# Kernel optimization log

Measured on AMD Instinct MI355X. Metric: run time of the kernel, lower is better.

## Reference

```python
import jax, jax.numpy as jnp
import numpy as np

B, H, W, D = 8, 32, 32, 384      # batch, height, width, channels (=dim)
E, HID, O = 8, 1536, 384         # num_experts, mlp hidden (dim*4), out_dim
TOP_K = 2


def setup_inputs() -> dict:
    key = jax.random.key(0)
    ks = jax.random.split(key, 5)
    x = jax.random.normal(ks[0], (B, H, W, D), dtype=jnp.float32)
    # router (noise_linear unused: eval path, train=False)
    Wg = 0.02 * jax.random.normal(ks[1], (D, E), dtype=jnp.float32)
    bg = jnp.zeros((E,), dtype=jnp.float32)
    # per-expert MLP params stacked along expert axis
    W1 = 0.02 * jax.random.normal(ks[2], (E, D, HID), dtype=jnp.float32)
    b1 = jnp.zeros((E, HID), dtype=jnp.float32)
    W2 = 0.02 * jax.random.normal(ks[3], (E, HID, O), dtype=jnp.float32)
    b2 = jnp.zeros((E, O), dtype=jnp.float32)
    return {"x": x, "Wg": Wg, "bg": bg, "W1": W1, "b1": b1, "W2": W2, "b2": b2}


def reference(x, Wg, bg, W1, b1, W2, b2):
    # --- NoisyTopkRouter (eval: train=False -> no noise branch) ---
    logits = jnp.einsum('bhwd,de->bhwe', x, Wg) + bg            # [B,H,W,E]
    _, top_idx = jax.lax.top_k(logits, TOP_K)                   # [B,H,W,K]
    # mask of selected experts; sparse logits = logits where selected, -inf else
    sel = jnp.sum(jax.nn.one_hot(top_idx, E, dtype=jnp.float32), axis=-2) > 0
    sparse_logits = jnp.where(sel, logits, -jnp.inf)
    gates = jax.nn.softmax(sparse_logits, axis=-1)              # zero on non-top-k

    # --- experts: since gate is exactly 0 off the top-k, the masked
    # gather-MLP-scatter loop equals a gate-weighted sum of all expert MLPs ---
    h = jnp.einsum('bhwd,edf->bhwef', x, W1) + b1               # [B,H,W,E,HID]
    h = jax.nn.gelu(h, approximate=False)                       # torch nn.GELU = exact
    y = jnp.einsum('bhwef,efo->bhweo', h, W2) + b2              # [B,H,W,E,O]
    out = jnp.einsum('bhweo,bhwe->bhwo', y, gates)              # [B,H,W,O]
    return out
```

## Files before the change

### kernel.cpp

```cpp
#include <hip/hip_runtime.h>
#include <cmath>

#define N_TOK 8192
#define DIM   384
#define NEXP  8
#define HID   1536
#define OUTD  384
#define CAP_MT 72
#define CAP_TOK 2304
#define CAP_TB 18

typedef __attribute__((ext_vector_type(8)))  __bf16 bf16x8;
typedef __attribute__((ext_vector_type(16))) float  f32x16;
typedef __attribute__((ext_vector_type(4)))  float  f32x4;
typedef __attribute__((ext_vector_type(8)))  unsigned short u16x8;

__device__ __forceinline__ unsigned short f2bf(float f) {
    unsigned u = __float_as_uint(f);
    u += 0x7FFF + ((u >> 16) & 1);
    return (unsigned short)(u >> 16);
}

__device__ __forceinline__ float bf2f(unsigned short s) {
    return __uint_as_float(((unsigned)s) << 16);
}

__device__ __forceinline__ float gelu_exact(float x) {
    return 0.5f * x * (1.0f + erff(x * 0.70710678118654752f));
}

__device__ __forceinline__ void cp16(const unsigned short* g, unsigned short* l) {
    __builtin_amdgcn_global_load_lds(
        (const __attribute__((address_space(1))) unsigned int*)g,
        (__attribute__((address_space(3))) unsigned int*)l, 16, 0, 0);
}

__global__ void swizzle_kernel(const float* __restrict__ W1, const float* __restrict__ W2,
                               unsigned short* __restrict__ w1s, unsigned short* __restrict__ w2s,
                               int* __restrict__ cnt) {
    if (blockIdx.x == 0 && threadIdx.x < NEXP) cnt[threadIdx.x] = 0;
    int gid = blockIdx.x * blockDim.x + threadIdx.x;
    const int T1 = NEXP * 48 * 24 * 64;
    const int T2 = NEXP * 12 * 96 * 64;
    const float* src; unsigned short* dst; int K, N, NT, KT, g;
    if (gid < T1)           { src = W1; dst = w1s; K = DIM; N = HID;  NT = 48; KT = 24; g = gid; }
    else if (gid < T1 + T2) { src = W2; dst = w2s; K = HID; N = OUTD; NT = 12; KT = 96; g = gid - T1; }
    else return;
    int l  = g & 63;
    int kt = (g >> 6) % KT;
    int nt = ((g >> 6) / KT) % NT;
    int e  = g / (64 * KT * NT);
    const float* s = src + ((size_t)e * K + kt * 16 + (l >> 5) * 8) * N + nt * 32 + (l & 31);
    unsigned short r[8];
    #pragma unroll
    for (int j = 0; j < 8; ++j) r[j] = f2bf(s[(size_t)j * N]);
    *(uint4*)(dst + (size_t)g * 8) = *(uint4*)r;
}

__global__ void router_kernel(const float* __restrict__ x, const float* __restrict__ Wg,
                              const float* __restrict__ bg, int* __restrict__ cnt,
                              int* __restrict__ btok, int* __restrict__ tokmap,
                              float* __restrict__ gmap) {
    __shared__ float WgL[NEXP * DIM];
    __shared__ int lcnt[NEXP];
    __shared__ int lbase[NEXP];
    int tid = threadIdx.x;
    for (int i = tid; i < DIM * NEXP; i += 256) {
        int ch = i >> 3, e = i & 7;
        WgL[e * DIM + ch] = Wg[i];
    }
    if (tid < NEXP) lcnt[tid] = 0;
    __syncthreads();

    int tl  = tid >> 3;
    int seg = tid & 7;
    int t   = blockIdx.x * 32 + tl;

    float lg[NEXP] = {0.f, 0.f, 0.f, 0.f, 0.f, 0.f, 0.f, 0.f};
    const float* xr = x + (size_t)t * DIM;
    #pragma unroll
    for (int d4 = 0; d4 < 12; ++d4) {
        float4 v = *(const float4*)(xr + d4 * 32 + seg * 4);
        #pragma unroll
        for (int e = 0; e < NEXP; ++e) {
            float4 w = *(const float4*)&WgL[e * DIM + d4 * 32 + seg * 4];
            lg[e] += v.x * w.x + v.y * w.y + v.z * w.z + v.w * w.w;
        }
    }
    #pragma unroll
    for (int off = 1; off < 8; off <<= 1)
        #pragma unroll
        for (int e = 0; e < NEXP; ++e)
            lg[e] += __shfl_xor(lg[e], off);

    int p0 = 0, p1 = 0, i0 = 0, i1 = 0;
    float g0 = 0.f, g1 = 0.f;
    if (seg == 0) {
        float v0 = -INFINITY, v1 = -INFINITY;
        #pragma unroll
        for (int e = 0; e < NEXP; ++e) {
            float v = lg[e] + bg[e];
            if (v > v0)      { v1 = v0; i1 = i0; v0 = v; i0 = e; }
            else if (v > v1) { v1 = v;  i1 = e; }
        }
        float e1 = expf(v1 - v0);
        g0 = 1.f / (1.f + e1);
        g1 = e1  / (1.f + e1);
        p0 = atomicAdd(&lcnt[i0], 1);
        p1 = atomicAdd(&lcnt[i1], 1);
    }
    __syncthreads();
    if (tid < NEXP) lbase[tid] = atomicAdd(&cnt[tid], lcnt[tid]);
    __syncthreads();
    if (seg == 0) {
        int o0 = lbase[i0] + p0, o1 = lbase[i1] + p1;
        btok[i0 * N_TOK + o0] = t;
        btok[i1 * N_TOK + o1] = t;
        ((int4*)tokmap)[t] = make_int4(i0, o0, i1, o1);
        ((float2*)gmap)[t] = make_float2(g0, g1);
    }
}

__global__ void gather_kernel(const float* __restrict__ x, const int* __restrict__ cnt,
                              const int* __restrict__ btok, unsigned short* __restrict__ xg) {
    int mt = blockIdx.x, e = blockIdx.y;
    int cntE = cnt[e];
    if (mt * 32 >= cntE) return;
    int tid = threadIdx.x;
    int m = tid & 31, kt0 = tid >> 5;
    int pos = mt * 32 + m;
    int idx = (pos < cntE) ? pos : cntE - 1;
    int tok = btok[e * N_TOK + idx];
    const float* xr = x + (size_t)tok * DIM;
    #pragma unroll
    for (int kk = 0; kk < 3; ++kk) {
        int kt = kt0 + kk * 8;
        #pragma unroll
        for (int kh = 0; kh < 2; ++kh) {
            float4 v0 = *(const float4*)(xr + kt * 16 + kh * 8);
            float4 v1 = *(const float4*)(xr + kt * 16 + kh * 8 + 4);
            unsigned short rr[8];
            rr[0] = f2bf(v0.x); rr[1] = f2bf(v0.y); rr[2] = f2bf(v0.z); rr[3] = f2bf(v0.w);
            rr[4] = f2bf(v1.x); rr[5] = f2bf(v1.y); rr[6] = f2bf(v1.z); rr[7] = f2bf(v1.w);
            *(uint4*)(xg + (size_t)(((e * CAP_MT + mt) * 24 + kt) * 64 + kh * 32 + m) * 8) =
                *(uint4*)rr;
        }
    }
}

__global__ __launch_bounds__(256, 3) void gemm1_kernel(
        const unsigned short* __restrict__ xg, const unsigned short* __restrict__ w1s,
        const float* __restrict__ b1, const int* __restrict__ cnt,
        unsigned short* __restrict__ h) {
    int L = blockIdx.x;
    int e = L & 7;
    int r = L >> 3;
    int nb = r % 12;
    int tb = r / 12;
    int cntE = cnt[e];
    if (tb * 128 >= cntE) return;

    __shared__ unsigned short stg[32 * 512];

    int tid = threadIdx.x;
    int wave = tid >> 6, lane = tid & 63;
    int m31 = lane & 31, kh = lane >> 5;
    int wm = wave & 1, wn = wave >> 1;

    f32x16 acc[2][2];
    #pragma unroll
    for (int i = 0; i < 2; ++i)
        #pragma unroll
        for (int j = 0; j < 2; ++j)
            acc[i][j] = (f32x16){0.f,0.f,0.f,0.f,0.f,0.f,0.f,0.f,0.f,0.f,0.f,0.f,0.f,0.f,0.f,0.f};

    const unsigned short* xa = xg  + ((size_t)(e * CAP_MT + tb * 4) * 24) * 512;
    const unsigned short* wb = w1s + ((size_t)(e * 48 + nb * 4) * 24) * 512;

    const unsigned short* sbase = (wave < 2)
        ? xa + ((size_t)(wave * 2) * 24) * 512 + lane * 8
        : wb + ((size_t)((wave - 2) * 2) * 24) * 512 + lane * 8;
    unsigned short* dbase = &stg[wave * 8 * 512];

    for (int ks = 0; ks < 6; ++ks) {
        __syncthreads();
        const unsigned short* sk = sbase + ks * 2048;
        #pragma unroll
        for (int q = 0; q < 8; ++q)
            cp16(sk + (q >> 2) * (24 * 512) + (q & 3) * 512, dbase + q * 512);
        __syncthreads();
        #pragma unroll
        for (int kt = 0; kt < 4; ++kt) {
            bf16x8 a0 = *(const bf16x8*)&stg[((wm * 2 + 0) * 4 + kt) * 512 + lane * 8];
            bf16x8 a1 = *(const bf16x8*)&stg[((wm * 2 + 1) * 4 + kt) * 512 + lane * 8];
            bf16x8 b0 = *(const bf16x8*)&stg[(16 + (wn * 2 + 0) * 4 + kt) * 512 + lane * 8];
            bf16x8 b1v = *(const bf16x8*)&stg[(16 + (wn * 2 + 1) * 4 + kt) * 512 + lane * 8];
            acc[0][0] = __builtin_amdgcn_mfma_f32_32x32x16_bf16(a0, b0,  acc[0][0], 0, 0, 0);
            acc[0][1] = __builtin_amdgcn_mfma_f32_32x32x16_bf16(a0, b1v, acc[0][1], 0, 0, 0);
            acc[1][0] = __builtin_amdgcn_mfma_f32_32x32x16_bf16(a1, b0,  acc[1][0], 0, 0, 0);
            acc[1][1] = __builtin_amdgcn_mfma_f32_32x32x16_bf16(a1, b1v, acc[1][1], 0, 0, 0);
        }
    }

    __syncthreads();
    char* hw = (char*)&stg[wave * 4096];
    float bv0 = b1[e * HID + nb * 128 + wn * 64 + m31];
    float bv1 = b1[e * HID + nb * 128 + wn * 64 + 32 + m31];
    #pragma unroll
    for (int im = 0; im < 2; ++im)
        #pragma unroll
        for (int in = 0; in < 2; ++in) {
            float bv = in ? bv1 : bv0;
            #pragma unroll
            for (int rr = 0; rr < 16; ++rr) {
                int row = im * 32 + (rr & 3) + 8 * (rr >> 2) + 4 * kh;
                int col = in * 32 + m31;
                unsigned boff = (unsigned)(row * 128 + col * 2) ^ ((row & 7) << 4);
                *(unsigned short*)(hw + boff) = f2bf(gelu_exact(acc[im][in][rr] + bv));
            }
        }
    #pragma unroll
    for (int mtl = 0; mtl < 2; ++mtl)
        #pragma unroll
        for (int ktl = 0; ktl < 4; ++ktl) {
            int rowl = mtl * 32 + m31;
            int coll = ktl * 16 + kh * 8;
            unsigned boff = (unsigned)(rowl * 128 + coll * 2) ^ ((rowl & 7) << 4);
            uint4 v = *(const uint4*)(hw + boff);
            int mt = tb * 4 + wm * 2 + mtl;
            int kt = nb * 8 + wn * 4 + ktl;
            *(uint4*)(h + ((size_t)((e * CAP_MT + mt) * 96 + kt)) * 512 + lane * 8) = v;
        }
}

__global__ __launch_bounds__(512, 4) void gemm2_kernel(
        const unsigned short* __restrict__ h, const unsigned short* __restrict__ w2s,
        const int* __restrict__ cnt, unsigned short* __restrict__ yp) {
    int L = blockIdx.x;
    int e = L & 7;
    int r = L >> 3;
    int nb = r % 3;
    int tb = r / 3;
    int cntE = cnt[e];
    if (tb * 128 >= cntE) return;

    __shared__ unsigned short stg[32 * 512];

    int tid = threadIdx.x;
    int wave = tid >> 6, lane = tid & 63;
    int m31 = lane & 31, kh = lane >> 5;
    int wm = wave & 1;
    int wn = wave >> 1;

    f32x16 acc[2];
    acc[0] = (f32x16){0.f,0.f,0.f,0.f,0.f,0.f,0.f,0.f,0.f,0.f,0.f,0.f,0.f,0.f,0.f,0.f};
    acc[1] = acc[0];

    const unsigned short* xa = h   + ((size_t)(e * CAP_MT + tb * 4) * 96) * 512;
    const unsigned short* wb = w2s + ((size_t)(e * 12 + nb * 4) * 96) * 512;

    const unsigned short* sbase = (wave < 4)
        ? xa + ((size_t)wave * 96) * 512 + lane * 8
        : wb + ((size_t)(wave - 4) * 96) * 512 + lane * 8;
    unsigned short* dbase = &stg[wave * 4 * 512];

    for (int ks = 0; ks < 24; ++ks) {
        __syncthreads();
        const unsigned short* sk = sbase + ks * 2048;
        #pragma unroll
        for (int q = 0; q < 4; ++q)
            cp16(sk + q * 512, dbase + q * 512);
        __syncthreads();
        #pragma unroll
        for (int kt = 0; kt < 4; ++kt) {
            bf16x8 b  = *(const bf16x8*)&stg[(16 + wn * 4 + kt) * 512 + lane * 8];
            bf16x8 a0 = *(const bf16x8*)&stg[((wm * 2 + 0) * 4 + kt) * 512 + lane * 8];
            bf16x8 a1 = *(const bf16x8*)&stg[((wm * 2 + 1) * 4 + kt) * 512 + lane * 8];
            acc[0] = __builtin_amdgcn_mfma_f32_32x32x16_bf16(a0, b, acc[0], 0, 0, 0);
            acc[1] = __builtin_amdgcn_mfma_f32_32x32x16_bf16(a1, b, acc[1], 0, 0, 0);
        }
    }

    __syncthreads();
    char* hw = (char*)&stg[wave * 2048];
    #pragma unroll
    for (int s = 0; s < 2; ++s)
        #pragma unroll
        for (int rr = 0; rr < 16; ++rr) {
            int rowl = s * 32 + (rr & 3) + 8 * (rr >> 2) + 4 * kh;
            *(unsigned short*)(hw + rowl * 64 + m31 * 2) = f2bf(acc[s][rr]);
        }
    #pragma unroll
    for (int it = 0; it < 4; ++it) {
        int rowl = it * 16 + (lane >> 2);
        int cc   = lane & 3;
        uint4 v = *(const uint4*)(hw + rowl * 64 + cc * 16);
        int pos = tb * 128 + wm * 64 + rowl;
        *(uint4*)(yp + (size_t)(e * CAP_TOK + pos) * OUTD + nb * 128 + wn * 32 + cc * 8) = v;
    }
}

__global__ void reduce_kernel(const unsigned short* __restrict__ yp,
                              const int* __restrict__ tokmap, const float* __restrict__ gmap,
                              const float* __restrict__ b2, float* __restrict__ out) {
    int gid = blockIdx.x * 256 + threadIdx.x;
    int t = gid / 48, q = gid - t * 48;
    int4   tm = ((const int4*)tokmap)[t];
    float2 g  = ((const float2*)gmap)[t];
    const unsigned short* p0 = yp + ((size_t)(tm.x * CAP_TOK + tm.y)) * OUTD + q * 8;
    const unsigned short* p1 = yp + ((size_t)(tm.z * CAP_TOK + tm.w)) * OUTD + q * 8;
    u16x8 a = __builtin_nontemporal_load((const u16x8*)p0);
    u16x8 b = __builtin_nontemporal_load((const u16x8*)p1);
    const float* c0 = &b2[tm.x * OUTD + q * 8];
    const float* c1 = &b2[tm.z * OUTD + q * 8];
    f32x4 r0, r1;
    #pragma unroll
    for (int j = 0; j < 4; ++j) {
        r0[j] = g.x * (bf2f(a[j]) + c0[j]) + g.y * (bf2f(b[j]) + c1[j]);
        r1[j] = g.x * (bf2f(a[4 + j]) + c0[4 + j]) + g.y * (bf2f(b[4 + j]) + c1[4 + j]);
    }
    float* op = &out[(size_t)t * OUTD + q * 8];
    __builtin_nontemporal_store(r0, (f32x4*)op);
    __builtin_nontemporal_store(r1, (f32x4*)(op + 4));
}

extern "C" void kernel_launch(void* const* d_in, const int* in_sizes, int n_in,
                              void* d_out, int out_size, void* d_ws, size_t ws_size,
                              hipStream_t stream) {
    const float* x  = (const float*)d_in[0];
    const float* Wg = (const float*)d_in[1];
    const float* bg = (const float*)d_in[2];
    const float* W1 = (const float*)d_in[3];
    const float* b1 = (const float*)d_in[4];
    const float* W2 = (const float*)d_in[5];
    const float* b2 = (const float*)d_in[6];
    float* out = (float*)d_out;

    char* ws = (char*)d_ws;
    int*            cnt    = (int*)ws;
    int*            btok   = (int*)(ws + 1024);
    int*            tokmap = (int*)(ws + 263168);
    float*          gmap   = (float*)(ws + 394240);
    unsigned short* xg     = (unsigned short*)(ws + 459776);
    unsigned short* w1s    = (unsigned short*)(ws + 14615552);
    unsigned short* w2s    = (unsigned short*)(ws + 24052736);
    unsigned short* h      = (unsigned short*)(ws + 33489920);
    unsigned short* yp     = xg;

    hipLaunchKernelGGL(swizzle_kernel, dim3(4608), dim3(256), 0, stream,
                       W1, W2, w1s, w2s, cnt);
    hipLaunchKernelGGL(router_kernel, dim3(N_TOK / 32), dim3(256), 0, stream,
                       x, Wg, bg, cnt, btok, tokmap, gmap);
    hipLaunchKernelGGL(gather_kernel, dim3(CAP_MT, NEXP), dim3(256), 0, stream,
                       x, cnt, btok, xg);
    hipLaunchKernelGGL(gemm1_kernel, dim3(NEXP * 12 * CAP_TB), dim3(256), 0, stream,
                       xg, w1s, b1, cnt, h);
    hipLaunchKernelGGL(gemm2_kernel, dim3(NEXP * 3 * CAP_TB), dim3(512), 0, stream,
                       h, w2s, cnt, yp);
    hipLaunchKernelGGL(reduce_kernel, dim3(N_TOK * 48 / 256), dim3(256), 0, stream,
                       yp, tokmap, gmap, b2, out);
}
```

Baseline: 182.3 us.

## Use 512-thread blocks and deeper K stages in both expert GEMMs

gemm1 moves from 4 waves with 2x2 MFMA tiles to 8 waves with 2x1 tiles, and loads 128-wide K chunks so it runs 3 stages instead of 6. gemm2 likewise doubles its K chunk per stage, from 24 stages to 12. The goal is fewer barriers per K and more waves to hide latency. In exchange, shared memory per block doubles to 64 KB, which may cut the number of resident blocks, and gemm1's per-wave A/B register reuse drops. gemm1's epilogue now uses a padded 80-byte row stride instead of the XOR swizzle.

```diff
diff --git a/kernel.cpp b/kernel.cpp
--- a/kernel.cpp
+++ b/kernel.cpp
@@ -148,7 +148,7 @@
     }
 }
 
-__global__ __launch_bounds__(256, 3) void gemm1_kernel(
+__global__ __launch_bounds__(512, 4) void gemm1_kernel(
         const unsigned short* __restrict__ xg, const unsigned short* __restrict__ w1s,
         const float* __restrict__ b1, const int* __restrict__ cnt,
         unsigned short* __restrict__ h) {
@@ -160,75 +160,60 @@
     int cntE = cnt[e];
     if (tb * 128 >= cntE) return;
 
-    __shared__ unsigned short stg[32 * 512];
+    __shared__ unsigned short stg[64 * 512];
 
     int tid = threadIdx.x;
     int wave = tid >> 6, lane = tid & 63;
     int m31 = lane & 31, kh = lane >> 5;
-    int wm = wave & 1, wn = wave >> 1;
-
-    f32x16 acc[2][2];
-    #pragma unroll
-    for (int i = 0; i < 2; ++i)
-        #pragma unroll
-        for (int j = 0; j < 2; ++j)
-            acc[i][j] = (f32x16){0.f,0.f,0.f,0.f,0.f,0.f,0.f,0.f,0.f,0.f,0.f,0.f,0.f,0.f,0.f,0.f};
+    int wm = wave & 1;
+    int wn = wave >> 1;
+
+    f32x16 acc[2];
+    acc[0] = (f32x16){0.f,0.f,0.f,0.f,0.f,0.f,0.f,0.f,0.f,0.f,0.f,0.f,0.f,0.f,0.f,0.f};
+    acc[1] = acc[0];
 
     const unsigned short* xa = xg  + ((size_t)(e * CAP_MT + tb * 4) * 24) * 512;
     const unsigned short* wb = w1s + ((size_t)(e * 48 + nb * 4) * 24) * 512;
 
-    const unsigned short* sbase = (wave < 2)
-        ? xa + ((size_t)(wave * 2) * 24) * 512 + lane * 8
-        : wb + ((size_t)((wave - 2) * 2) * 24) * 512 + lane * 8;
+    const unsigned short* sbase = (wave < 4)
+        ? xa + ((size_t)wave * 24) * 512 + lane * 8
+        : wb + ((size_t)(wave - 4) * 24) * 512 + lane * 8;
     unsigned short* dbase = &stg[wave * 8 * 512];
 
-    for (int ks = 0; ks < 6; ++ks) {
+    for (int ks = 0; ks < 3; ++ks) {
         __syncthreads();
-        const unsigned short* sk = sbase + ks * 2048;
+        const unsigned short* sk = sbase + ks * 4096;
         #pragma unroll
         for (int q = 0; q < 8; ++q)
-            cp16(sk + (q >> 2) * (24 * 512) + (q & 3) * 512, dbase + q * 512);
+            cp16(sk + q * 512, dbase + q * 512);
         __syncthreads();
         #pragma unroll
-        for (int kt = 0; kt < 4; ++kt) {
-            bf16x8 a0 = *(const bf16x8*)&stg[((wm * 2 + 0) * 4 + kt) * 512 + lane * 8];
-            bf16x8 a1 = *(const bf16x8*)&stg[((wm * 2 + 1) * 4 + kt) * 512 + lane * 8];
-            bf16x8 b0 = *(const bf16x8*)&stg[(16 + (wn * 2 + 0) * 4 + kt) * 512 + lane * 8];
-            bf16x8 b1v = *(const bf16x8*)&stg[(16 + (wn * 2 + 1) * 4 + kt) * 512 + lane * 8];
-            acc[0][0] = __builtin_amdgcn_mfma_f32_32x32x16_bf16(a0, b0,  acc[0][0], 0, 0, 0);
-            acc[0][1] = __builtin_amdgcn_mfma_f32_32x32x16_bf16(a0, b1v, acc[0][1], 0, 0, 0);
-            acc[1][0] = __builtin_amdgcn_mfma_f32_32x32x16_bf16(a1, b0,  acc[1][0], 0, 0, 0);
-            acc[1][1] = __builtin_amdgcn_mfma_f32_32x32x16_bf16(a1, b1v, acc[1][1], 0, 0, 0);
-        }
-    }
-
-    __syncthreads();
-    char* hw = (char*)&stg[wave * 4096];
-    float bv0 = b1[e * HID + nb * 128 + wn * 64 + m31];
-    float bv1 = b1[e * HID + nb * 128 + wn * 64 + 32 + m31];
-    #pragma unroll
-    for (int im = 0; im < 2; ++im)
-        #pragma unroll
-        for (int in = 0; in < 2; ++in) {
-            float bv = in ? bv1 : bv0;
-            #pragma unroll
-            for (int rr = 0; rr < 16; ++rr) {
-                int row = im * 32 + (rr & 3) + 8 * (rr >> 2) + 4 * kh;
-                int col = in * 32 + m31;
-                unsigned boff = (unsigned)(row * 128 + col * 2) ^ ((row & 7) << 4);
-                *(unsigned short*)(hw + boff) = f2bf(gelu_exact(acc[im][in][rr] + bv));
-            }
+        for (int kt = 0; kt < 8; ++kt) {
+            bf16x8 b  = *(const bf16x8*)&stg[(32 + wn * 8 + kt) * 512 + lane * 8];
+            bf16x8 a0 = *(const bf16x8*)&stg[((wm * 2 + 0) * 8 + kt) * 512 + lane * 8];
+            bf16x8 a1 = *(const bf16x8*)&stg[((wm * 2 + 1) * 8 + kt) * 512 + lane * 8];
+            acc[0] = __builtin_amdgcn_mfma_f32_32x32x16_bf16(a0, b, acc[0], 0, 0, 0);
+            acc[1] = __builtin_amdgcn_mfma_f32_32x32x16_bf16(a1, b, acc[1], 0, 0, 0);
+        }
+    }
+
+    __syncthreads();
+    char* hw = (char*)stg + wave * 5120;
+    float bv = b1[e * HID + nb * 128 + wn * 32 + m31];
+    #pragma unroll
+    for (int s = 0; s < 2; ++s)
+        #pragma unroll
+        for (int rr = 0; rr < 16; ++rr) {
+            int rowl = s * 32 + (rr & 3) + 8 * (rr >> 2) + 4 * kh;
+            *(unsigned short*)(hw + rowl * 80 + m31 * 2) = f2bf(gelu_exact(acc[s][rr] + bv));
         }
     #pragma unroll
     for (int mtl = 0; mtl < 2; ++mtl)
         #pragma unroll
-        for (int ktl = 0; ktl < 4; ++ktl) {
-            int rowl = mtl * 32 + m31;
-            int coll = ktl * 16 + kh * 8;
-            unsigned boff = (unsigned)(rowl * 128 + coll * 2) ^ ((rowl & 7) << 4);
-            uint4 v = *(const uint4*)(hw + boff);
+        for (int ktl = 0; ktl < 2; ++ktl) {
+            uint4 v = *(const uint4*)(hw + (mtl * 32 + m31) * 80 + (ktl * 16 + kh * 8) * 2);
             int mt = tb * 4 + wm * 2 + mtl;
-            int kt = nb * 8 + wn * 4 + ktl;
+            int kt = nb * 8 + wn * 2 + ktl;
             *(uint4*)(h + ((size_t)((e * CAP_MT + mt) * 96 + kt)) * 512 + lane * 8) = v;
         }
 }
@@ -244,7 +229,7 @@
     int cntE = cnt[e];
     if (tb * 128 >= cntE) return;
 
-    __shared__ unsigned short stg[32 * 512];
+    __shared__ unsigned short stg[64 * 512];
 
     int tid = threadIdx.x;
     int wave = tid >> 6, lane = tid & 63;
@@ -262,27 +247,27 @@
     const unsigned short* sbase = (wave < 4)
         ? xa + ((size_t)wave * 96) * 512 + lane * 8
         : wb + ((size_t)(wave - 4) * 96) * 512 + lane * 8;
-    unsigned short* dbase = &stg[wave * 4 * 512];
-
-    for (int ks = 0; ks < 24; ++ks) {
+    unsigned short* dbase = &stg[wave * 8 * 512];
+
+    for (int ks = 0; ks < 12; ++ks) {
         __syncthreads();
-        const unsigned short* sk = sbase + ks * 2048;
-        #pragma unroll
-        for (int q = 0; q < 4; ++q)
+        const unsigned short* sk = sbase + ks * 4096;
+        #pragma unroll
+        for (int q = 0; q < 8; ++q)
             cp16(sk + q * 512, dbase + q * 512);
         __syncthreads();
         #pragma unroll
-        for (int kt = 0; kt < 4; ++kt) {
-            bf16x8 b  = *(const bf16x8*)&stg[(16 + wn * 4 + kt) * 512 + lane * 8];
-            bf16x8 a0 = *(const bf16x8*)&stg[((wm * 2 + 0) * 4 + kt) * 512 + lane * 8];
-            bf16x8 a1 = *(const bf16x8*)&stg[((wm * 2 + 1) * 4 + kt) * 512 + lane * 8];
+        for (int kt = 0; kt < 8; ++kt) {
+            bf16x8 b  = *(const bf16x8*)&stg[(32 + wn * 8 + kt) * 512 + lane * 8];
+            bf16x8 a0 = *(const bf16x8*)&stg[((wm * 2 + 0) * 8 + kt) * 512 + lane * 8];
+            bf16x8 a1 = *(const bf16x8*)&stg[((wm * 2 + 1) * 8 + kt) * 512 + lane * 8];
             acc[0] = __builtin_amdgcn_mfma_f32_32x32x16_bf16(a0, b, acc[0], 0, 0, 0);
             acc[1] = __builtin_amdgcn_mfma_f32_32x32x16_bf16(a1, b, acc[1], 0, 0, 0);
         }
     }
 
     __syncthreads();
-    char* hw = (char*)&stg[wave * 2048];
+    char* hw = (char*)stg + wave * 4096;
     #pragma unroll
     for (int s = 0; s < 2; ++s)
         #pragma unroll
@@ -353,7 +338,7 @@
                        x, Wg, bg, cnt, btok, tokmap, gmap);
     hipLaunchKernelGGL(gather_kernel, dim3(CAP_MT, NEXP), dim3(256), 0, stream,
                        x, cnt, btok, xg);
-    hipLaunchKernelGGL(gemm1_kernel, dim3(NEXP * 12 * CAP_TB), dim3(256), 0, stream,
+    hipLaunchKernelGGL(gemm1_kernel, dim3(NEXP * 12 * CAP_TB), dim3(512), 0, stream,
                        xg, w1s, b1, cnt, h);
     hipLaunchKernelGGL(gemm2_kernel, dim3(NEXP * 3 * CAP_TB), dim3(512), 0, stream,
                        h, w2s, cnt, yp);
```

After: 181.0 us. No clear change (-0.7%).
